# Performance work log

Measured on AMD Instinct MI355X. Metric: run time of the kernel, lower is better.

The kernel has to match this reference:

```python
import jax, jax.numpy as jnp
import numpy as np

N_PATCHES = 14
PS = 16            # patch size: 224 / 14
C, H_IMG, W_IMG = 3, 224, 224
HIDDEN = 768
HEADS = 12
DH = HIDDEN // HEADS
BLOCKS = 12
MLP = 4 * HIDDEN
OUT = 1000
SEQ = N_PATCHES ** 2 + 1  # 197
BATCH = 64


def get_positional_embeddings(seq_len, d):
    # sin(i/10000^(j/d)) for even j, cos(i/10000^((j-1)/d)) for odd j
    i = jnp.arange(seq_len, dtype=jnp.float32)[:, None]
    j = jnp.arange(d)[None, :]
    even = (j % 2 == 0)
    expo = jnp.where(even, j, j - 1).astype(jnp.float32) / d
    ang = i / (10000.0 ** expo)
    return jnp.where(even, jnp.sin(ang), jnp.cos(ang))


def layernorm(x, g, b, eps=1e-5):
    mu = x.mean(-1, keepdims=True)
    var = ((x - mu) ** 2).mean(-1, keepdims=True)
    return (x - mu) / jnp.sqrt(var + eps) * g + b


def mhsa(x, qw, qb, kw, kb, vw, vb):
    # x: [B,S,HIDDEN]; per-head linears qw/kw/vw: [H,DH,DH] (torch Linear weight layout)
    B, S, _ = x.shape
    xh = x.reshape(B, S, HEADS, DH)
    q = jnp.einsum('bshd,hed->bshe', xh, qw) + qb
    k = jnp.einsum('bshd,hed->bshe', xh, kw) + kb
    v = jnp.einsum('bshd,hed->bshe', xh, vw) + vb
    scores = jnp.einsum('bshe,bthe->bhst', q, k) / jnp.sqrt(jnp.float32(DH))
    attn = jax.nn.softmax(scores, axis=-1)
    out = jnp.einsum('bhst,bthe->bshe', attn, v)
    return out.reshape(B, S, HIDDEN)


def vit_block(x, p):
    ln1_g, ln1_b, qw, qb, kw, kb, vw, vb, ln2_g, ln2_b, w1, b1, w2, b2 = p
    x = x + mhsa(layernorm(x, ln1_g, ln1_b), qw, qb, kw, kb, vw, vb)
    h = layernorm(x, ln2_g, ln2_b)
    h = jax.nn.gelu(h @ w1.T + b1, approximate=False) @ w2.T + b2
    return x + h


def patchify(images):
    # [N,C,H,W] -> [N, n_patches^2, C*PS*PS], channel-major within each patch
    n = images.shape[0]
    x = images.reshape(n, C, N_PATCHES, PS, N_PATCHES, PS)
    x = x.transpose(0, 2, 4, 1, 3, 5)  # n, pi, pj, c, ps, ps
    return x.reshape(n, N_PATCHES * N_PATCHES, C * PS * PS)


def setup_inputs() -> dict:
    key = jax.random.key(0)
    ks = jax.random.split(key, 20)
    s = 0.02
    return {
        'images': jax.random.normal(ks[0], (BATCH, C, H_IMG, W_IMG), jnp.float32),
        'mapper_w': jax.random.normal(ks[1], (HIDDEN, C * PS * PS), jnp.float32) * s,
        'mapper_b': jnp.zeros((HIDDEN,), jnp.float32),
        'cls_token': jax.random.uniform(ks[2], (1, HIDDEN), jnp.float32),
        'ln1_g': jnp.ones((BLOCKS, HIDDEN), jnp.float32),
        'ln1_b': jnp.zeros((BLOCKS, HIDDEN), jnp.float32),
        'qw': jax.random.normal(ks[3], (BLOCKS, HEADS, DH, DH), jnp.float32) * s,
        'qb': jnp.zeros((BLOCKS, HEADS, DH), jnp.float32),
        'kw': jax.random.normal(ks[4], (BLOCKS, HEADS, DH, DH), jnp.float32) * s,
        'kb': jnp.zeros((BLOCKS, HEADS, DH), jnp.float32),
        'vw': jax.random.normal(ks[5], (BLOCKS, HEADS, DH, DH), jnp.float32) * s,
        'vb': jnp.zeros((BLOCKS, HEADS, DH), jnp.float32),
        'ln2_g': jnp.ones((BLOCKS, HIDDEN), jnp.float32),
        'ln2_b': jnp.zeros((BLOCKS, HIDDEN), jnp.float32),
        'w1': jax.random.normal(ks[6], (BLOCKS, MLP, HIDDEN), jnp.float32) * s,
        'b1': jnp.zeros((BLOCKS, MLP), jnp.float32),
        'w2': jax.random.normal(ks[7], (BLOCKS, HIDDEN, MLP), jnp.float32) * s,
        'b2': jnp.zeros((BLOCKS, HIDDEN), jnp.float32),
        'head_w': jax.random.normal(ks[8], (OUT, HIDDEN), jnp.float32) * s,
        'head_b': jnp.zeros((OUT,), jnp.float32),
    }


def reference(images, mapper_w, mapper_b, cls_token, ln1_g, ln1_b, qw, qb, kw, kb,
              vw, vb, ln2_g, ln2_b, w1, b1, w2, b2, head_w, head_b):
    n = images.shape[0]
    patches = patchify(images)
    tokens = patches @ mapper_w.T + mapper_b                      # [B, 196, HIDDEN]
    cls = jnp.broadcast_to(cls_token[None], (n, 1, HIDDEN))
    tokens = jnp.concatenate([cls, tokens], axis=1)               # [B, 197, HIDDEN]
    out = tokens + get_positional_embeddings(SEQ, HIDDEN)[None]

    stacked = (ln1_g, ln1_b, qw, qb, kw, kb, vw, vb, ln2_g, ln2_b, w1, b1, w2, b2)

    def step(x, p):
        return vit_block(x, p), None

    out, _ = jax.lax.scan(step, out, stacked)
    cls_out = out[:, 0]                                           # [B, HIDDEN]
    return jax.nn.softmax(cls_out @ head_w.T + head_b, axis=-1)
```

## Files before the change

kernel.cpp:

```cpp
#include <hip/hip_runtime.h>
#include <cstdint>
#include <cstddef>
#include <cstdio>

using u16 = unsigned short;
using u32 = unsigned int;

typedef __attribute__((ext_vector_type(8))) __bf16 bf16x8;
typedef __attribute__((ext_vector_type(4))) float f32x4;

struct alignas(16) U128 { u32 w[4]; };
struct alignas(16) F4   { float x[4]; };
struct alignas(8)  US4  { u16 h[4]; };

#define DEVFN static __device__ __forceinline__

DEVFN u16 f2bf(float x) {
  union { float f; u32 u; } v; v.f = x;
  u32 r = v.u + 0x7fffu + ((v.u >> 16) & 1u);
  return (u16)(r >> 16);
}

DEVFN bf16x8 ld16(const u16* p) { return __builtin_bit_cast(bf16x8, *(const U128*)p); }

DEVFN f32x4 mfma16(bf16x8 a, bf16x8 b, f32x4 c) {
  return __builtin_amdgcn_mfma_f32_16x16x32_bf16(a, b, c, 0, 0, 0);
}

DEVFN void gload_lds16(const u16* g, u16* l) {
  __builtin_amdgcn_global_load_lds(
      (const __attribute__((address_space(1))) void*)g,
      (__attribute__((address_space(3))) void*)l, 16, 0, 0);
}

DEVFN float gelu(float x) {
  float z = fabsf(x) * 0.70710678118f;
  float t = __builtin_amdgcn_rcpf(1.f + 0.3275911f * z);
  float p = t * (0.254829592f + t * (-0.284496736f + t * (1.421413741f +
            t * (-1.453152027f + t * 1.061405429f))));
  float e = __expf(-z * z);
  float erfz = 1.f - p * e;
  erfz = copysignf(erfz, x);
  return 0.5f * x * (1.f + erfz);
}

DEVFN void remap_bid(int bid, int Mb, int Nb, int& bm, int& bn) {
  const int ngrp  = Mb >> 3;
  const int per   = Nb << 3;
  const int nfull = ngrp * per;
  if (bid < nfull) {
    const int bmg = bid / per;
    const int rem = bid - bmg * per;
    bn = rem >> 3;
    bm = (bmg << 3) + (rem & 7);
  } else {
    const int r = bid - nfull;
    const int q = r / Nb;
    bm = (ngrp << 3) + q;
    bn = r - q * Nb;
  }
}

constexpr int SEQL   = 197;
constexpr int NB     = 64;
constexpr int NH     = 12;
constexpr int MROWS  = NB * SEQL;
constexpr int MPAD   = 12672;
constexpr int MPAD2  = 12800;
constexpr int MPATCH = NB * 196;
constexpr int SP     = 208;
constexpr int SP2    = 224;
constexpr int BHN    = NB * NH;

constexpr size_t OFF_X    = 0;
constexpr size_t OFF_ALN  = OFF_X    + (size_t)MPAD * 768 * 4;
constexpr size_t OFF_H    = OFF_ALN  + (size_t)MPAD2 * 768 * 2;
constexpr size_t OFF_WQKV = OFF_H    + (size_t)MPAD2 * 3072 * 2;
constexpr size_t OFF_W1   = OFF_WQKV + (size_t)2304 * 128 * 2;
constexpr size_t OFF_W2   = OFF_W1   + (size_t)3072 * 768 * 2;
constexpr size_t OFF_WMAP = OFF_W2   + (size_t)3072 * 768 * 2;
constexpr size_t OFF_Q    = OFF_WMAP + (size_t)768 * 768 * 2;
constexpr size_t OFF_K    = OFF_Q    + (size_t)BHN * SP * 64 * 2;
constexpr size_t OFF_VT   = OFF_K    + (size_t)BHN * SP * 64 * 2;
constexpr size_t OFF_PAT  = OFF_VT   + (size_t)BHN * 64 * SP2 * 2;
constexpr size_t OFF_POS  = OFF_PAT  + (size_t)MPATCH * 768 * 2;
constexpr size_t WS_NEED  = OFF_POS  + (size_t)SEQL * 768 * 4;

__global__ void zero_kernel(u32* __restrict__ p, long n) {
  long i = (long)blockIdx.x * 256 + threadIdx.x;
  long stride = (long)gridDim.x * 256;
  for (; i < n; i += stride) p[i] = 0u;
}

__global__ void cvt_kernel(const float* __restrict__ src, u16* __restrict__ dst, int n) {
  int i = blockIdx.x * 256 + threadIdx.x;
  if (i < n) dst[i] = f2bf(src[i]);
}

__global__ void pos_kernel(float* __restrict__ pos) {
  int i = blockIdx.x * 256 + threadIdx.x;
  if (i >= SEQL * 768) return;
  int s = i / 768, j = i - s * 768;
  float expo = (float)(j & ~1) * (1.0f / 768.0f);
  float ang  = (float)s * expf(-expo * logf(10000.0f));
  pos[i] = (j & 1) ? cosf(ang) : sinf(ang);
}

__global__ void cls_kernel(const float* __restrict__ cls, const float* __restrict__ pos,
                           float* __restrict__ X) {
  int b = blockIdx.x;
  for (int c = threadIdx.x; c < 768; c += 256)
    X[(size_t)b * SEQL * 768 + c] = cls[c] + pos[c];
}

__global__ void patchify_kernel(const float* __restrict__ img, u16* __restrict__ out) {
  int i = blockIdx.x * 256 + threadIdx.x;
  if (i >= MPATCH * 768) return;
  int m = i / 768, k = i - m * 768;
  int b = m / 196, p = m - b * 196;
  int py = p / 14, px = p - py * 14;
  int c = k >> 8, rem = k & 255, iy = rem >> 4, ix = rem & 15;
  float v = img[(((size_t)b * 3 + c) * 224 + py * 16 + iy) * 224 + px * 16 + ix];
  out[i] = f2bf(v);
}

__global__ void prep_kernel(const float* __restrict__ qw, const float* __restrict__ kw,
                            const float* __restrict__ vw, const float* __restrict__ w1,
                            const float* __restrict__ w2,
                            u16* __restrict__ Wqkv, u16* __restrict__ W1b,
                            u16* __restrict__ W2b, int blk) {
  const int NQ = 2304 * 128;
  const int N1 = 3072 * 768;
  int i = blockIdx.x * 256 + threadIdx.x;
  if (i < NQ) {
    int n = i >> 7, kk = i & 127;
    int p = n / 768, ef = n - p * 768;
    int h = ef >> 6, e = ef & 63;
    float v = 0.f;
    if ((kk >> 6) == (h & 1)) {
      int d = kk & 63;
      const float* w = (p == 0) ? qw : (p == 1) ? kw : vw;
      v = w[(((size_t)blk * NH + h) * 64 + e) * 64 + d];
    }
    Wqkv[i] = f2bf(v);
  } else if (i < NQ + N1) {
    int j = i - NQ;
    W1b[j] = f2bf(w1[(size_t)blk * N1 + j]);
  } else if (i < NQ + 2 * N1) {
    int j = i - NQ - N1;
    W2b[j] = f2bf(w2[(size_t)blk * N1 + j]);
  }
}

__global__ __launch_bounds__(256) void ln_kernel(const float* __restrict__ X,
    const float* __restrict__ g, const float* __restrict__ b, u16* __restrict__ out) {
  int row  = blockIdx.x * 4 + (threadIdx.x >> 6);
  int lane = threadIdx.x & 63;
  const float* x = X + (size_t)row * 768 + lane * 12;
  F4 a0 = *(const F4*)(x);
  F4 a1 = *(const F4*)(x + 4);
  F4 a2 = *(const F4*)(x + 8);
  float v[12];
  #pragma unroll
  for (int j = 0; j < 4; ++j) { v[j] = a0.x[j]; v[4 + j] = a1.x[j]; v[8 + j] = a2.x[j]; }
  float s = 0.f, q = 0.f;
  #pragma unroll
  for (int j = 0; j < 12; ++j) { s += v[j]; q += v[j] * v[j]; }
  #pragma unroll
  for (int d = 1; d < 64; d <<= 1) { s += __shfl_xor(s, d); q += __shfl_xor(q, d); }
  float mu  = s * (1.f / 768.f);
  float var = q * (1.f / 768.f) - mu * mu;
  float rs  = rsqrtf(var + 1e-5f);
  const float* gp = g + lane * 12;
  const float* bp = b + lane * 12;
  u16* op = out + (size_t)row * 768 + lane * 12;
  u16 o[12];
  #pragma unroll
  for (int j = 0; j < 12; ++j) o[j] = f2bf((v[j] - mu) * rs * gp[j] + bp[j]);
  #pragma unroll
  for (int c = 0; c < 3; ++c) {
    US4 w; w.h[0] = o[c*4]; w.h[1] = o[c*4+1]; w.h[2] = o[c*4+2]; w.h[3] = o[c*4+3];
    *(US4*)(op + c * 4) = w;
  }
}

enum { EPI_PATCH = 0, EPI_QKV = 1, EPI_GELU = 2, EPI_RESID = 3 };

template<int EPI>
__global__ __launch_bounds__(256, 3) void gemm128(
    const u16* __restrict__ A, const u16* __restrict__ B, int K, int lda, int ldb,
    int Mb, int Nb,
    const float* __restrict__ e0, const float* __restrict__ e1, const float* __restrict__ e2,
    float* __restrict__ f0, const float* __restrict__ f1,
    u16* __restrict__ o0, u16* __restrict__ o1, u16* __restrict__ o2) {
  __shared__ u16 Ab[3][128 * 32];
  __shared__ u16 Bb[3][128 * 32];
  const int tid  = threadIdx.x;
  const int wave = tid >> 6, lane = tid & 63;
  int bm, bn;
  remap_bid(blockIdx.x, Mb, Nb, bm, bn);
  const int fr = lane & 15, fg = lane >> 4;
  const int srow = wave * 16 + (lane >> 2);
  const int gcol = ((lane & 3) ^ ((lane >> 3) & 3)) * 8;
  const u16* gA = A + (size_t)(bm * 128 + srow) * lda + gcol;
  const u16* gB = B + (size_t)(bn * 128 + srow) * ldb + gcol;
  const int wm = (wave >> 1) * 64, wn = (wave & 1) * 64;
  const int sl = (fg ^ ((fr >> 1) & 3)) * 8;
  const int nt = K >> 5;

  auto STAGE = [&](int c, int t) {
    gload_lds16(gA + t * 32,                    &Ab[c][0] + wave * 512);
    gload_lds16(gA + t * 32 + (size_t)64 * lda, &Ab[c][0] + wave * 512 + 2048);
    gload_lds16(gB + t * 32,                    &Bb[c][0] + wave * 512);
    gload_lds16(gB + t * 32 + (size_t)64 * ldb, &Bb[c][0] + wave * 512 + 2048);
  };

  f32x4 acc[4][4] = {};
  STAGE(0, 0);
  if (nt > 1) STAGE(1, 1);
  int bi = 0;
  for (int t = 0; t < nt; ++t) {
    if (t + 1 < nt) asm volatile("s_waitcnt vmcnt(4)" ::: "memory");
    else            asm volatile("s_waitcnt vmcnt(0)" ::: "memory");
    __builtin_amdgcn_s_barrier();
    if (t + 2 < nt) { int si = bi + 2; if (si >= 3) si -= 3; STAGE(si, t + 2); }
    const u16* ab   = &Ab[bi][0];
    const u16* bbuf = &Bb[bi][0];
    bf16x8 af[4], bfv[4];
    #pragma unroll
    for (int i = 0; i < 4; ++i) af[i]  = ld16(ab + (wm + i * 16 + fr) * 32 + sl);
    #pragma unroll
    for (int j = 0; j < 4; ++j) bfv[j] = ld16(bbuf + (wn + j * 16 + fr) * 32 + sl);
    __builtin_amdgcn_s_setprio(1);
    #pragma unroll
    for (int i = 0; i < 4; ++i)
      #pragma unroll
      for (int j = 0; j < 4; ++j)
        acc[i][j] = mfma16(af[i], bfv[j], acc[i][j]);
    __builtin_amdgcn_s_setprio(0);
    bi = (bi + 1 == 3) ? 0 : bi + 1;
  }

  #pragma unroll
  for (int i = 0; i < 4; ++i) {
    #pragma unroll
    for (int r = 0; r < 4; ++r) {
      const int m = bm * 128 + wm + i * 16 + fg * 4 + r;
      if constexpr (EPI == EPI_PATCH) {
        const int bb = m / 196;
        const int s  = m - bb * 196 + 1;
        float* xrow = f0 + ((size_t)bb * SEQL + s) * 768;
        const float* prow = f1 + (size_t)s * 768;
        #pragma unroll
        for (int j = 0; j < 4; ++j) {
          const int n = bn * 128 + wn + j * 16 + fr;
          xrow[n] = acc[i][j][r] + e0[n] + prow[n];
        }
      } else if constexpr (EPI == EPI_GELU) {
        u16* hrow = o0 + (size_t)m * 3072;
        #pragma unroll
        for (int j = 0; j < 4; ++j) {
          const int n = bn * 128 + wn + j * 16 + fr;
          hrow[n] = f2bf(gelu(acc[i][j][r] + e0[n]));
        }
      } else {
        if (m < MROWS) {
          float* xrow = f0 + (size_t)m * 768;
          #pragma unroll
          for (int j = 0; j < 4; ++j) {
            const int n = bn * 128 + wn + j * 16 + fr;
            xrow[n] += acc[i][j][r] + e0[n];
          }
        }
      }
    }
  }
}

__global__ __launch_bounds__(256, 2) void qkv_gemm(
    const u16* __restrict__ A, const u16* __restrict__ B,
    const float* __restrict__ e0, const float* __restrict__ e1, const float* __restrict__ e2,
    u16* __restrict__ o0, u16* __restrict__ o1, u16* __restrict__ o2) {
  __shared__ u16 Ab[4][128 * 32];
  __shared__ u16 Bb[4][128 * 32];
  const int tid = threadIdx.x, wave = tid >> 6, lane = tid & 63;
  int bm, bn;
  remap_bid(blockIdx.x, MPAD / 128, 18, bm, bn);
  const int fr = lane & 15, fg = lane >> 4;
  const u16* Aw = A + (bn % 6) * 128;
  const int srow = wave * 16 + (lane >> 2);
  const int gcol = ((lane & 3) ^ ((lane >> 3) & 3)) * 8;
  const u16* gA = Aw + (size_t)(bm * 128 + srow) * 768 + gcol;
  const u16* gB = B + (size_t)(bn * 128 + srow) * 128 + gcol;
  const int wm = (wave >> 1) * 64, wn = (wave & 1) * 64;
  const int sl = (fg ^ ((fr >> 1) & 3)) * 8;

  #pragma unroll
  for (int c = 0; c < 4; ++c) {
    gload_lds16(gA + c * 32,                    &Ab[c][0] + wave * 512);
    gload_lds16(gA + c * 32 + (size_t)64 * 768, &Ab[c][0] + wave * 512 + 2048);
    gload_lds16(gB + c * 32,                    &Bb[c][0] + wave * 512);
    gload_lds16(gB + c * 32 + (size_t)64 * 128, &Bb[c][0] + wave * 512 + 2048);
  }
  asm volatile("s_waitcnt vmcnt(0)" ::: "memory");
  __builtin_amdgcn_s_barrier();

  f32x4 acc[4][4] = {};
  #pragma unroll
  for (int c = 0; c < 4; ++c) {
    bf16x8 af[4], bfv[4];
    #pragma unroll
    for (int i = 0; i < 4; ++i) af[i]  = ld16(&Ab[c][0] + (wm + i * 16 + fr) * 32 + sl);
    #pragma unroll
    for (int j = 0; j < 4; ++j) bfv[j] = ld16(&Bb[c][0] + (wn + j * 16 + fr) * 32 + sl);
    __builtin_amdgcn_s_setprio(1);
    #pragma unroll
    for (int i = 0; i < 4; ++i)
      #pragma unroll
      for (int j = 0; j < 4; ++j)
        acc[i][j] = mfma16(af[i], bfv[j], acc[i][j]);
    __builtin_amdgcn_s_setprio(0);
  }

  #pragma unroll
  for (int i = 0; i < 4; ++i) {
    #pragma unroll
    for (int r = 0; r < 4; ++r) {
      const int m = bm * 128 + wm + i * 16 + fg * 4 + r;
      if (m < MROWS) {
        const int bb = m / 197;
        const int s  = m - bb * 197;
        #pragma unroll
        for (int j = 0; j < 4; ++j) {
          const int n = bn * 128 + wn + j * 16 + fr;
          const int p = n / 768;
          const int ef = n - p * 768;
          const int h = ef >> 6, e = ef & 63;
          const size_t bh = (size_t)bb * NH + h;
          if (p == 0)      o0[(bh * SP + s) * 64 + e] = f2bf((acc[i][j][r] + e0[ef]) * 0.125f);
          else if (p == 1) o1[(bh * SP + s) * 64 + e] = f2bf(acc[i][j][r] + e1[ef]);
          else             o2[(bh * 64 + e) * SP2 + s] = f2bf(acc[i][j][r] + e2[ef]);
        }
      }
    }
  }
}

__global__ __launch_bounds__(256, 2) void attn_kernel(const u16* __restrict__ Q,
    const u16* __restrict__ Km, const u16* __restrict__ Vt, float* __restrict__ X) {
  __shared__ u16  P[4][16 * SP2];
  __shared__ u16  Kl[208 * 72];
  __shared__ float sums[4][16];
  const int bh = blockIdx.x;
  const int b = bh / NH, h = bh - b * NH;
  const int wave = threadIdx.x >> 6, lane = threadIdx.x & 63;
  const int fr = lane & 15, fg = lane >> 4;
  const u16* Qb = Q  + (size_t)bh * SP * 64;
  const u16* Kb = Km + (size_t)bh * SP * 64;
  const u16* Vb = Vt + (size_t)bh * 64 * SP2;
  {
    const int r0 = threadIdx.x >> 2;
    const int e  = (threadIdx.x & 3) * 16;
    #pragma unroll
    for (int rr = r0; rr < 208; rr += 64)
      *(U128*)(Kl + rr * 72 + e) = *(const U128*)(Kb + (size_t)rr * 64 + e);
  }
  __syncthreads();
  u16* Pl = &P[wave][0];
  for (int qt = wave; qt < 13; qt += 4) {
    const int s0 = qt * 16;
    bf16x8 qf0 = ld16(Qb + (size_t)(s0 + fr) * 64 + fg * 8);
    bf16x8 qf1 = ld16(Qb + (size_t)(s0 + fr) * 64 + 32 + fg * 8);
    f32x4 sc[13];
    #pragma unroll
    for (int tf = 0; tf < 13; ++tf) {
      f32x4 a = {0.f, 0.f, 0.f, 0.f};
      bf16x8 k0 = ld16(Kl + (tf * 16 + fr) * 72 + fg * 8);
      bf16x8 k1 = ld16(Kl + (tf * 16 + fr) * 72 + 32 + fg * 8);
      a = mfma16(qf0, k0, a);
      a = mfma16(qf1, k1, a);
      sc[tf] = a;
    }
    float mx[4] = {-3e38f, -3e38f, -3e38f, -3e38f};
    #pragma unroll
    for (int tf = 0; tf < 13; ++tf) {
      const bool ok = (tf * 16 + fr) < 197;
      #pragma unroll
      for (int r = 0; r < 4; ++r) {
        float v = ok ? sc[tf][r] : -3e38f;
        sc[tf][r] = v;
        mx[r] = fmaxf(mx[r], v);
      }
    }
    #pragma unroll
    for (int r = 0; r < 4; ++r)
      #pragma unroll
      for (int d = 1; d < 16; d <<= 1) mx[r] = fmaxf(mx[r], __shfl_xor(mx[r], d));
    float sm[4] = {0.f, 0.f, 0.f, 0.f};
    #pragma unroll
    for (int tf = 0; tf < 13; ++tf) {
      #pragma unroll
      for (int r = 0; r < 4; ++r) {
        float e = __expf(sc[tf][r] - mx[r]);
        sm[r] += e;
        Pl[(fg * 4 + r) * SP2 + tf * 16 + fr] = f2bf(e);
      }
    }
    #pragma unroll
    for (int r = 0; r < 4; ++r) {
      #pragma unroll
      for (int d = 1; d < 16; d <<= 1) sm[r] += __shfl_xor(sm[r], d);
      if (fr == 0) sums[wave][fg * 4 + r] = sm[r];
    }
    #pragma unroll
    for (int r = 0; r < 4; ++r) Pl[(fg * 4 + r) * SP2 + 208 + fr] = 0;
    f32x4 o[4] = {};
    #pragma unroll
    for (int ks = 0; ks < 7; ++ks) {
      bf16x8 pf = ld16(Pl + fr * SP2 + ks * 32 + fg * 8);
      #pragma unroll
      for (int ef = 0; ef < 4; ++ef) {
        bf16x8 vf = ld16(Vb + (size_t)(ef * 16 + fr) * SP2 + ks * 32 + fg * 8);
        o[ef] = mfma16(vf, pf, o[ef]);
      }
    }
    const float inv = 1.f / sums[wave][fr];
    const int s = s0 + fr;
    if (s < 197) {
      float* xp = X + ((size_t)b * SEQL + s) * 768 + h * 64;
      #pragma unroll
      for (int ef = 0; ef < 4; ++ef)
        #pragma unroll
        for (int r = 0; r < 4; ++r)
          xp[ef * 16 + fg * 4 + r] += o[ef][r] * inv;
    }
  }
}

__global__ __launch_bounds__(256) void head_kernel(const float* __restrict__ X,
    const float* __restrict__ hw, const float* __restrict__ hb, float* __restrict__ out) {
  __shared__ float xr[768];
  __shared__ float lg[1000];
  __shared__ float red[8];
  const int b = blockIdx.x, tid = threadIdx.x;
  for (int c = tid; c < 768; c += 256) xr[c] = X[(size_t)b * SEQL * 768 + c];
  __syncthreads();
  for (int n = tid; n < 1000; n += 256) {
    const F4* w4 = (const F4*)(hw + (size_t)n * 768);
    const F4* x4 = (const F4*)xr;
    float acc = hb[n];
    for (int k = 0; k < 192; ++k) {
      F4 w = w4[k]; F4 xv = x4[k];
      acc += w.x[0] * xv.x[0] + w.x[1] * xv.x[1] + w.x[2] * xv.x[2] + w.x[3] * xv.x[3];
    }
    lg[n] = acc;
  }
  __syncthreads();
  float m = -3e38f;
  for (int n = tid; n < 1000; n += 256) m = fmaxf(m, lg[n]);
  #pragma unroll
  for (int d = 1; d < 64; d <<= 1) m = fmaxf(m, __shfl_xor(m, d));
  if ((tid & 63) == 0) red[tid >> 6] = m;
  __syncthreads();
  m = fmaxf(fmaxf(red[0], red[1]), fmaxf(red[2], red[3]));
  float s = 0.f;
  for (int n = tid; n < 1000; n += 256) s += expf(lg[n] - m);
  #pragma unroll
  for (int d = 1; d < 64; d <<= 1) s += __shfl_xor(s, d);
  if ((tid & 63) == 0) red[4 + (tid >> 6)] = s;
  __syncthreads();
  s = red[4] + red[5] + red[6] + red[7];
  const float inv = 1.f / s;
  for (int n = tid; n < 1000; n += 256) out[(size_t)b * 1000 + n] = expf(lg[n] - m) * inv;
}

extern "C" void kernel_launch(void* const* d_in, const int* in_sizes, int n_in,
                              void* d_out, int out_size, void* d_ws, size_t ws_size,
                              hipStream_t stream) {
  (void)in_sizes; (void)n_in; (void)out_size;
  if (ws_size < WS_NEED) { printf("ws too small: %zu < %zu\n", ws_size, WS_NEED); return; }

  const float* images   = (const float*)d_in[0];
  const float* mapper_w = (const float*)d_in[1];
  const float* mapper_b = (const float*)d_in[2];
  const float* cls_tok  = (const float*)d_in[3];
  const float* ln1_g    = (const float*)d_in[4];
  const float* ln1_b    = (const float*)d_in[5];
  const float* qw       = (const float*)d_in[6];
  const float* qb       = (const float*)d_in[7];
  const float* kw       = (const float*)d_in[8];
  const float* kb       = (const float*)d_in[9];
  const float* vw       = (const float*)d_in[10];
  const float* vb       = (const float*)d_in[11];
  const float* ln2_g    = (const float*)d_in[12];
  const float* ln2_b    = (const float*)d_in[13];
  const float* w1       = (const float*)d_in[14];
  const float* b1       = (const float*)d_in[15];
  const float* w2       = (const float*)d_in[16];
  const float* b2       = (const float*)d_in[17];
  const float* head_w   = (const float*)d_in[18];
  const float* head_b   = (const float*)d_in[19];

  char* ws = (char*)d_ws;
  float* X    = (float*)(ws + OFF_X);
  u16*  Aln   = (u16*)(ws + OFF_ALN);
  u16*  Hb    = (u16*)(ws + OFF_H);
  u16*  Wqkv  = (u16*)(ws + OFF_WQKV);
  u16*  W1b   = (u16*)(ws + OFF_W1);
  u16*  W2b   = (u16*)(ws + OFF_W2);
  u16*  Wmap  = (u16*)(ws + OFF_WMAP);
  u16*  Qb    = (u16*)(ws + OFF_Q);
  u16*  Kb    = (u16*)(ws + OFF_K);
  u16*  Vtb   = (u16*)(ws + OFF_VT);
  u16*  Pat   = (u16*)(ws + OFF_PAT);
  float* Pos  = (float*)(ws + OFF_POS);

  zero_kernel<<<2048, 256, 0, stream>>>((u32*)Qb,  (long)(BHN * SP * 64 / 2));
  zero_kernel<<<2048, 256, 0, stream>>>((u32*)Kb,  (long)(BHN * SP * 64 / 2));
  zero_kernel<<<2048, 256, 0, stream>>>((u32*)Vtb, (long)(BHN * 64 * SP2 / 2));
  zero_kernel<<<64,   256, 0, stream>>>((u32*)(X + (size_t)MROWS * 768), (long)((MPAD - MROWS) * 768));

  pos_kernel<<<(SEQL * 768 + 255) / 256, 256, 0, stream>>>(Pos);
  cvt_kernel<<<(768 * 768 + 255) / 256, 256, 0, stream>>>(mapper_w, Wmap, 768 * 768);
  patchify_kernel<<<(MPATCH * 768 + 255) / 256, 256, 0, stream>>>(images, Pat);
  cls_kernel<<<NB, 256, 0, stream>>>(cls_tok, Pos, X);

  gemm128<EPI_PATCH><<<(MPATCH / 128) * (768 / 128), 256, 0, stream>>>(
      Pat, Wmap, 768, 768, 768, MPATCH / 128, 768 / 128,
      mapper_b, nullptr, nullptr, X, Pos, nullptr, nullptr, nullptr);

  const int PREP_N = 2304 * 128 + 2 * 3072 * 768;
  for (int blk = 0; blk < 12; ++blk) {
    ln_kernel<<<MPAD / 4, 256, 0, stream>>>(X, ln1_g + blk * 768, ln1_b + blk * 768, Aln);
    prep_kernel<<<(PREP_N + 255) / 256, 256, 0, stream>>>(
        qw, kw, vw, w1, w2, Wqkv, W1b, W2b, blk);
    qkv_gemm<<<(MPAD / 128) * 18, 256, 0, stream>>>(
        Aln, Wqkv, qb + blk * 768, kb + blk * 768, vb + blk * 768, Qb, Kb, Vtb);
    attn_kernel<<<BHN, 256, 0, stream>>>(Qb, Kb, Vtb, X);
    ln_kernel<<<MPAD / 4, 256, 0, stream>>>(X, ln2_g + blk * 768, ln2_b + blk * 768, Aln);
    gemm128<EPI_GELU><<<(MPAD / 128) * (3072 / 128), 256, 0, stream>>>(
        Aln, W1b, 768, 768, 768, MPAD / 128, 3072 / 128,
        b1 + blk * 3072, nullptr, nullptr, nullptr, nullptr, Hb, nullptr, nullptr);
    gemm128<EPI_RESID><<<(MPAD / 128) * (768 / 128), 256, 0, stream>>>(
        Hb, W2b, 3072, 3072, 3072, MPAD / 128, 768 / 128,
        b2 + blk * 768, nullptr, nullptr, X, nullptr, nullptr, nullptr, nullptr);
  }

  head_kernel<<<NB, 256, 0, stream>>>(X, head_w, head_b, (float*)d_out);
}
```

Measured before the change: 4.181 ms.

## Vectorize epilogue stores via swapped MFMA operands, single-buffer gemm128, vectorize prep

Swaps the MFMA operand order so each lane holds four consecutive output columns, which lets the gemm128, qkv and attention epilogues use 16-byte and 8-byte vector loads and stores instead of scalar ones. The prep kernel now converts the w1/w2 weights four elements at a time. Separately, gemm128 drops its three-stage LDS pipeline for a single buffer with two syncthreads per K step and raises the occupancy hint from 3 to 5. The smaller LDS footprint is meant to allow more resident blocks, but global loads no longer overlap with MFMA work, so the main GEMMs may stall on memory latency.

```diff
diff --git a/kernel.cpp b/kernel.cpp
--- a/kernel.cpp
+++ b/kernel.cpp
@@ -130,7 +130,7 @@
                             u16* __restrict__ Wqkv, u16* __restrict__ W1b,
                             u16* __restrict__ W2b, int blk) {
   const int NQ = 2304 * 128;
-  const int N1 = 3072 * 768;
+  const int NV = 3072 * 768 / 4;
   int i = blockIdx.x * 256 + threadIdx.x;
   if (i < NQ) {
     int n = i >> 7, kk = i & 127;
@@ -143,12 +143,20 @@
       v = w[(((size_t)blk * NH + h) * 64 + e) * 64 + d];
     }
     Wqkv[i] = f2bf(v);
-  } else if (i < NQ + N1) {
-    int j = i - NQ;
-    W1b[j] = f2bf(w1[(size_t)blk * N1 + j]);
-  } else if (i < NQ + 2 * N1) {
-    int j = i - NQ - N1;
-    W2b[j] = f2bf(w2[(size_t)blk * N1 + j]);
+  } else if (i < NQ + NV) {
+    int j = (i - NQ) * 4;
+    F4 v = *(const F4*)(w1 + (size_t)blk * 3072 * 768 + j);
+    US4 o;
+    #pragma unroll
+    for (int r = 0; r < 4; ++r) o.h[r] = f2bf(v.x[r]);
+    *(US4*)(W1b + j) = o;
+  } else if (i < NQ + 2 * NV) {
+    int j = (i - NQ - NV) * 4;
+    F4 v = *(const F4*)(w2 + (size_t)blk * 3072 * 768 + j);
+    US4 o;
+    #pragma unroll
+    for (int r = 0; r < 4; ++r) o.h[r] = f2bf(v.x[r]);
+    *(US4*)(W2b + j) = o;
   }
 }
 
@@ -187,14 +195,14 @@
 enum { EPI_PATCH = 0, EPI_QKV = 1, EPI_GELU = 2, EPI_RESID = 3 };
 
 template<int EPI>
-__global__ __launch_bounds__(256, 3) void gemm128(
+__global__ __launch_bounds__(256, 5) void gemm128(
     const u16* __restrict__ A, const u16* __restrict__ B, int K, int lda, int ldb,
     int Mb, int Nb,
     const float* __restrict__ e0, const float* __restrict__ e1, const float* __restrict__ e2,
     float* __restrict__ f0, const float* __restrict__ f1,
     u16* __restrict__ o0, u16* __restrict__ o1, u16* __restrict__ o2) {
-  __shared__ u16 Ab[3][128 * 32];
-  __shared__ u16 Bb[3][128 * 32];
+  __shared__ u16 Ab[128 * 32];
+  __shared__ u16 Bb[128 * 32];
   const int tid  = threadIdx.x;
   const int wave = tid >> 6, lane = tid & 63;
   int bm, bn;
@@ -208,69 +216,68 @@
   const int sl = (fg ^ ((fr >> 1) & 3)) * 8;
   const int nt = K >> 5;
 
-  auto STAGE = [&](int c, int t) {
-    gload_lds16(gA + t * 32,                    &Ab[c][0] + wave * 512);
-    gload_lds16(gA + t * 32 + (size_t)64 * lda, &Ab[c][0] + wave * 512 + 2048);
-    gload_lds16(gB + t * 32,                    &Bb[c][0] + wave * 512);
-    gload_lds16(gB + t * 32 + (size_t)64 * ldb, &Bb[c][0] + wave * 512 + 2048);
-  };
-
   f32x4 acc[4][4] = {};
-  STAGE(0, 0);
-  if (nt > 1) STAGE(1, 1);
-  int bi = 0;
   for (int t = 0; t < nt; ++t) {
-    if (t + 1 < nt) asm volatile("s_waitcnt vmcnt(4)" ::: "memory");
-    else            asm volatile("s_waitcnt vmcnt(0)" ::: "memory");
-    __builtin_amdgcn_s_barrier();
-    if (t + 2 < nt) { int si = bi + 2; if (si >= 3) si -= 3; STAGE(si, t + 2); }
-    const u16* ab   = &Ab[bi][0];
-    const u16* bbuf = &Bb[bi][0];
+    gload_lds16(gA + t * 32,                    Ab + wave * 512);
+    gload_lds16(gA + t * 32 + (size_t)64 * lda, Ab + wave * 512 + 2048);
+    gload_lds16(gB + t * 32,                    Bb + wave * 512);
+    gload_lds16(gB + t * 32 + (size_t)64 * ldb, Bb + wave * 512 + 2048);
+    __syncthreads();
     bf16x8 af[4], bfv[4];
     #pragma unroll
-    for (int i = 0; i < 4; ++i) af[i]  = ld16(ab + (wm + i * 16 + fr) * 32 + sl);
-    #pragma unroll
-    for (int j = 0; j < 4; ++j) bfv[j] = ld16(bbuf + (wn + j * 16 + fr) * 32 + sl);
+    for (int i = 0; i < 4; ++i) af[i]  = ld16(Ab + (wm + i * 16 + fr) * 32 + sl);
+    #pragma unroll
+    for (int j = 0; j < 4; ++j) bfv[j] = ld16(Bb + (wn + j * 16 + fr) * 32 + sl);
     __builtin_amdgcn_s_setprio(1);
     #pragma unroll
     for (int i = 0; i < 4; ++i)
       #pragma unroll
       for (int j = 0; j < 4; ++j)
-        acc[i][j] = mfma16(af[i], bfv[j], acc[i][j]);
+        acc[i][j] = mfma16(bfv[j], af[i], acc[i][j]);
     __builtin_amdgcn_s_setprio(0);
-    bi = (bi + 1 == 3) ? 0 : bi + 1;
+    __syncthreads();
   }
 
   #pragma unroll
   for (int i = 0; i < 4; ++i) {
-    #pragma unroll
-    for (int r = 0; r < 4; ++r) {
-      const int m = bm * 128 + wm + i * 16 + fg * 4 + r;
-      if constexpr (EPI == EPI_PATCH) {
-        const int bb = m / 196;
-        const int s  = m - bb * 196 + 1;
-        float* xrow = f0 + ((size_t)bb * SEQL + s) * 768;
-        const float* prow = f1 + (size_t)s * 768;
+    const int m = bm * 128 + wm + i * 16 + fr;
+    if constexpr (EPI == EPI_PATCH) {
+      const int bb = m / 196;
+      const int s  = m - bb * 196 + 1;
+      float* xrow = f0 + ((size_t)bb * SEQL + s) * 768;
+      const float* prow = f1 + (size_t)s * 768;
+      #pragma unroll
+      for (int j = 0; j < 4; ++j) {
+        const int n0 = bn * 128 + wn + j * 16 + fg * 4;
+        F4 pz = *(const F4*)(prow + n0);
+        F4 bz = *(const F4*)(e0 + n0);
+        F4 o;
+        #pragma unroll
+        for (int r = 0; r < 4; ++r) o.x[r] = acc[i][j][r] + bz.x[r] + pz.x[r];
+        *(F4*)(xrow + n0) = o;
+      }
+    } else if constexpr (EPI == EPI_GELU) {
+      u16* hrow = o0 + (size_t)m * 3072;
+      #pragma unroll
+      for (int j = 0; j < 4; ++j) {
+        const int n0 = bn * 128 + wn + j * 16 + fg * 4;
+        F4 bz = *(const F4*)(e0 + n0);
+        US4 w;
+        #pragma unroll
+        for (int r = 0; r < 4; ++r) w.h[r] = f2bf(gelu(acc[i][j][r] + bz.x[r]));
+        *(US4*)(hrow + n0) = w;
+      }
+    } else {
+      if (m < MROWS) {
+        float* xrow = f0 + (size_t)m * 768;
         #pragma unroll
         for (int j = 0; j < 4; ++j) {
-          const int n = bn * 128 + wn + j * 16 + fr;
-          xrow[n] = acc[i][j][r] + e0[n] + prow[n];
-        }
-      } else if constexpr (EPI == EPI_GELU) {
-        u16* hrow = o0 + (size_t)m * 3072;
-        #pragma unroll
-        for (int j = 0; j < 4; ++j) {
-          const int n = bn * 128 + wn + j * 16 + fr;
-          hrow[n] = f2bf(gelu(acc[i][j][r] + e0[n]));
-        }
-      } else {
-        if (m < MROWS) {
-          float* xrow = f0 + (size_t)m * 768;
+          const int n0 = bn * 128 + wn + j * 16 + fg * 4;
+          F4 x = *(const F4*)(xrow + n0);
+          F4 bz = *(const F4*)(e0 + n0);
           #pragma unroll
-          for (int j = 0; j < 4; ++j) {
-            const int n = bn * 128 + wn + j * 16 + fr;
-            xrow[n] += acc[i][j][r] + e0[n];
-          }
+          for (int r = 0; r < 4; ++r) x.x[r] += acc[i][j][r] + bz.x[r];
+          *(F4*)(xrow + n0) = x;
         }
       }
     }
@@ -279,7 +286,7 @@
 
 __global__ __launch_bounds__(256, 2) void qkv_gemm(
     const u16* __restrict__ A, const u16* __restrict__ B,
-    const float* __restrict__ e0, const float* __restrict__ e1, const float* __restrict__ e2,
+    const float* __restrict__ eq, const float* __restrict__ ek, const float* __restrict__ ev,
     u16* __restrict__ o0, u16* __restrict__ o1, u16* __restrict__ o2) {
   __shared__ u16 Ab[4][128 * 32];
   __shared__ u16 Bb[4][128 * 32];
@@ -318,28 +325,37 @@
     for (int i = 0; i < 4; ++i)
       #pragma unroll
       for (int j = 0; j < 4; ++j)
-        acc[i][j] = mfma16(af[i], bfv[j], acc[i][j]);
+        acc[i][j] = mfma16(bfv[j], af[i], acc[i][j]);
     __builtin_amdgcn_s_setprio(0);
   }
 
   #pragma unroll
   for (int i = 0; i < 4; ++i) {
-    #pragma unroll
-    for (int r = 0; r < 4; ++r) {
-      const int m = bm * 128 + wm + i * 16 + fg * 4 + r;
-      if (m < MROWS) {
-        const int bb = m / 197;
-        const int s  = m - bb * 197;
-        #pragma unroll
-        for (int j = 0; j < 4; ++j) {
-          const int n = bn * 128 + wn + j * 16 + fr;
-          const int p = n / 768;
-          const int ef = n - p * 768;
-          const int h = ef >> 6, e = ef & 63;
-          const size_t bh = (size_t)bb * NH + h;
-          if (p == 0)      o0[(bh * SP + s) * 64 + e] = f2bf((acc[i][j][r] + e0[ef]) * 0.125f);
-          else if (p == 1) o1[(bh * SP + s) * 64 + e] = f2bf(acc[i][j][r] + e1[ef]);
-          else             o2[(bh * 64 + e) * SP2 + s] = f2bf(acc[i][j][r] + e2[ef]);
+    const int m = bm * 128 + wm + i * 16 + fr;
+    if (m < MROWS) {
+      const int bb = m / 197;
+      const int s  = m - bb * 197;
+      #pragma unroll
+      for (int j = 0; j < 4; ++j) {
+        const int n0 = bn * 128 + wn + j * 16 + fg * 4;
+        const int p  = n0 / 768;
+        const int ef = n0 - p * 768;
+        const int h  = ef >> 6, e = ef & 63;
+        const size_t bh = (size_t)bb * NH + h;
+        if (p == 0) {
+          US4 w;
+          #pragma unroll
+          for (int r = 0; r < 4; ++r) w.h[r] = f2bf((acc[i][j][r] + eq[ef + r]) * 0.125f);
+          *(US4*)(o0 + (bh * SP + s) * 64 + e) = w;
+        } else if (p == 1) {
+          US4 w;
+          #pragma unroll
+          for (int r = 0; r < 4; ++r) w.h[r] = f2bf(acc[i][j][r] + ek[ef + r]);
+          *(US4*)(o1 + (bh * SP + s) * 64 + e) = w;
+        } else {
+          #pragma unroll
+          for (int r = 0; r < 4; ++r)
+            o2[(bh * 64 + e + r) * SP2 + s] = f2bf(acc[i][j][r] + ev[ef + r]);
         }
       }
     }
@@ -429,10 +445,12 @@
     if (s < 197) {
       float* xp = X + ((size_t)b * SEQL + s) * 768 + h * 64;
       #pragma unroll
-      for (int ef = 0; ef < 4; ++ef)
+      for (int ef = 0; ef < 4; ++ef) {
+        F4 x = *(const F4*)(xp + ef * 16 + fg * 4);
         #pragma unroll
-        for (int r = 0; r < 4; ++r)
-          xp[ef * 16 + fg * 4 + r] += o[ef][r] * inv;
+        for (int r = 0; r < 4; ++r) x.x[r] += o[ef][r] * inv;
+        *(F4*)(xp + ef * 16 + fg * 4) = x;
+      }
     }
   }
 }
@@ -529,7 +547,7 @@
       Pat, Wmap, 768, 768, 768, MPATCH / 128, 768 / 128,
       mapper_b, nullptr, nullptr, X, Pos, nullptr, nullptr, nullptr);
 
-  const int PREP_N = 2304 * 128 + 2 * 3072 * 768;
+  const int PREP_N = 2304 * 128 + 2 * (3072 * 768 / 4);
   for (int blk = 0; blk < 12; ++blk) {
     ln_kernel<<<MPAD / 4, 256, 0, stream>>>(X, ln1_g + blk * 768, ln1_b + blk * 768, Aln);
     prep_kernel<<<(PREP_N + 255) / 256, 256, 0, stream>>>(
```

Result: slower. 8.675 ms (+107.5%).
